# Optimization experiments

Measured on AMD Instinct MI355X. Metric: run time of the kernel, lower is better.

The kernel has to match this reference:

```python
import jax, jax.numpy as jnp
import numpy as np
import math

BS, SEQ, EMBED = 1, 2048, 512
N_HEADS, FEAT = 8, 64
W, DILATION = 32, 4


def setup_inputs() -> dict:
    key = jax.random.key(0)
    ks = jax.random.split(key, 8)
    s = 0.02
    return {
        "x": jax.random.normal(ks[0], (BS, SEQ, EMBED), dtype=jnp.float32),
        "Wq": jax.random.normal(ks[1], (EMBED, N_HEADS * FEAT), dtype=jnp.float32) * s,
        "Wk": jax.random.normal(ks[2], (EMBED, N_HEADS * FEAT), dtype=jnp.float32) * s,
        "Wv": jax.random.normal(ks[3], (EMBED, N_HEADS * FEAT), dtype=jnp.float32) * s,
        "Wff1": jax.random.normal(ks[4], (EMBED, EMBED), dtype=jnp.float32) * s,
        "bff1": jnp.zeros((EMBED,), dtype=jnp.float32),
        "Wff2": jax.random.normal(ks[5], (EMBED, EMBED), dtype=jnp.float32) * s,
        "bff2": jnp.zeros((EMBED,), dtype=jnp.float32),
    }


def reference(x, Wq, Wk, Wv, Wff1, bff1, Wff2, bff2):
    bs, seq, embed = x.shape
    sqrt_d = math.sqrt(FEAT)

    def proj_heads(W):
        # (bs, seq, embed) @ (embed, h*f) -> (bs, h, seq, f)
        h = jnp.einsum('bse,ef->bsf', x, W)
        return h.reshape(bs, seq, N_HEADS, FEAT).transpose(0, 2, 1, 3)

    q = proj_heads(Wq)
    k = proj_heads(Wk)
    v = proj_heads(Wv)

    pad = W * DILATION
    pad_k = jnp.pad(k, ((0, 0), (0, 0), (pad, pad), (0, 0)))
    pad_v = jnp.pad(v, ((0, 0), (0, 0), (pad, pad), (0, 0)))

    # dilated window indices into the padded sequence: (seq, 2W+1)
    idx = jnp.arange(seq)[:, None] + jnp.arange(0, 2 * W * DILATION + 1, DILATION)[None, :]

    diag_k = pad_k[:, :, idx, :]               # (bs, h, seq, 2W+1, f)
    attn = jnp.einsum('bhsf,bhskf->bhsk', q, diag_k)
    # Faithful to source: softmax first, THEN divide by sqrt(d)
    attn = jax.nn.softmax(attn, axis=-1) / sqrt_d
    diag_v = pad_v[:, :, idx, :]               # (bs, h, seq, 2W+1, f)
    ctx = jnp.einsum('bhsk,bhskf->bhsf', attn, diag_v)

    x_attn = ctx.transpose(0, 2, 1, 3).reshape(bs, seq, embed)
    f = jax.nn.relu(x_attn @ Wff1 + bff1)
    g = jax.nn.relu(f @ Wff2 + bff2)
    return x_attn + g
```

## Files before the change

kernel.cpp:

```cpp
#include <hip/hip_runtime.h>
#include <hip/hip_bf16.h>

#define SEQ 2048
#define EMB 512

typedef __attribute__((ext_vector_type(8))) short short8;
typedef __attribute__((ext_vector_type(4))) float f32x4;

__device__ __forceinline__ ushort f2b(float f) {
    union { __hip_bfloat16 h; ushort u; } cv;
    cv.h = __float2bfloat16(f);
    return cv.u;
}

__device__ __forceinline__ void async_copy16(const void* g, void* l) {
    __builtin_amdgcn_global_load_lds(
        (const __attribute__((address_space(1))) void*)g,
        (__attribute__((address_space(3))) void*)l, 16, 0, 0);
}

__global__ __launch_bounds__(256)
void cvt_x(const float* __restrict__ x, ushort* __restrict__ xb) {
    int i = (blockIdx.x * 256 + threadIdx.x) * 4;
    float4 v = *(const float4*)(x + i);
    ushort4 o;
    o.x = f2b(v.x); o.y = f2b(v.y); o.z = f2b(v.z); o.w = f2b(v.w);
    *(ushort4*)(xb + i) = o;
}

__global__ __launch_bounds__(256)
void transpose_w(const float* W0, const float* W1, const float* W2,
                 const float* W3, const float* W4,
                 ushort* T0, ushort* T1, ushort* T2, ushort* T3, ushort* T4) {
    const float* W; ushort* T;
    switch (blockIdx.z) {
        case 0: W = W0; T = T0; break;
        case 1: W = W1; T = T1; break;
        case 2: W = W2; T = T2; break;
        case 3: W = W3; T = T3; break;
        default: W = W4; T = T4; break;
    }
    __shared__ float t[32][33];
    const int n0 = blockIdx.x * 32, k0 = blockIdx.y * 32;
    const int tx = threadIdx.x, ty = threadIdx.y;
    for (int r = ty; r < 32; r += 8)
        t[r][tx] = W[(k0 + r) * 512 + n0 + tx];
    __syncthreads();
    for (int r = ty; r < 32; r += 8)
        T[(n0 + r) * 512 + k0 + tx] = f2b(t[tx][r]);
}

template<bool BIAS, bool RELU, bool ADDSRC, bool OUTBF16>
__global__ __launch_bounds__(256)
void gemm_bt(const ushort* __restrict__ A, const ushort* __restrict__ BT,
             const float* __restrict__ bias, const float* __restrict__ addsrc,
             void* __restrict__ C, int ldc)
{
    __shared__ __align__(16) ushort As[2][64][64];
    __shared__ __align__(16) ushort Bs[2][64][64];
    const int tid = threadIdx.x;
    const int wv = tid >> 6, lane = tid & 63;
    const int lane15 = lane & 15, quad = lane >> 4;
    const int n0 = blockIdx.x * 64, m0 = blockIdx.y * 64;
    const int wm = wv & 1, wn = wv >> 1;
    const int srow = lane >> 3;
    const int soct = lane & 7;

    f32x4 acc[2][2];
    const f32x4 z4 = {0.f, 0.f, 0.f, 0.f};
    acc[0][0] = z4; acc[0][1] = z4; acc[1][0] = z4; acc[1][1] = z4;

    auto stage = [&](int buf, int kc) {
        #pragma unroll
        for (int half = 0; half < 2; ++half) {
            int r0 = wv * 16 + half * 8;
            int r  = r0 + srow;
            int g  = soct ^ (r & 7);
            async_copy16(A + (size_t)(m0 + r) * 512 + kc * 64 + g * 8,
                         &As[buf][r0][0]);
            async_copy16(BT + (size_t)(n0 + r) * 512 + kc * 64 + g * 8,
                         &Bs[buf][r0][0]);
        }
    };
    auto compute = [&](int buf) {
        #pragma unroll
        for (int ks = 0; ks < 2; ++ks) {
            short8 a[2], b[2];
            const int oct = ((ks * 4 + quad) ^ (lane15 & 7)) * 8;
            #pragma unroll
            for (int mi = 0; mi < 2; ++mi)
                a[mi] = *(const short8*)&As[buf][wm * 32 + mi * 16 + lane15][oct];
            #pragma unroll
            for (int ni = 0; ni < 2; ++ni)
                b[ni] = *(const short8*)&Bs[buf][wn * 32 + ni * 16 + lane15][oct];
            #pragma unroll
            for (int mi = 0; mi < 2; ++mi)
                #pragma unroll
                for (int ni = 0; ni < 2; ++ni)
                    acc[mi][ni] = __builtin_amdgcn_mfma_f32_16x16x32_bf16(
                        a[mi], b[ni], acc[mi][ni], 0, 0, 0);
        }
    };

    stage(0, 0);
    __syncthreads();
    for (int kc = 0; kc < 8; ++kc) {
        if (kc < 7) stage((kc + 1) & 1, kc + 1);
        compute(kc & 1);
        __syncthreads();
    }

    #pragma unroll
    for (int mi = 0; mi < 2; ++mi)
        #pragma unroll
        for (int ni = 0; ni < 2; ++ni)
            #pragma unroll
            for (int reg = 0; reg < 4; ++reg) {
                int row = m0 + wm * 32 + mi * 16 + quad * 4 + reg;
                int col = n0 + wn * 32 + ni * 16 + lane15;
                float v = acc[mi][ni][reg];
                if (BIAS) v += bias[col];
                if (RELU) v = fmaxf(v, 0.f);
                if (ADDSRC) v += addsrc[(size_t)row * ldc + col];
                if (OUTBF16) ((ushort*)C)[(size_t)row * ldc + col] = f2b(v);
                else         ((float*)C)[(size_t)row * ldc + col] = v;
            }
}

__global__ __launch_bounds__(256)
void vt_transpose(const ushort* __restrict__ QKVb, ushort* __restrict__ Vtg)
{
    const int sb = blockIdx.x, h = blockIdx.y;
    const int s0 = sb * 64;
    const int tid = threadIdx.x;
    __shared__ ushort tile[64][72];
    #pragma unroll
    for (int it = 0; it < 2; ++it) {
        int row = (tid >> 3) + 32 * it;
        int o = tid & 7;
        *(short8*)&tile[row][o * 8] =
            *(const short8*)&QKVb[(size_t)(s0 + row) * 1536 + 1024 + h * 64 + o * 8];
    }
    __syncthreads();
    const int f = tid >> 2, r = tid & 3;
    ushort tmp[16];
    #pragma unroll
    for (int k = 0; k < 16; ++k) tmp[k] = tile[4 * k + r][f];
    size_t base = (((size_t)h * 4 + r) * 64 + f) * 512 + s0 / 4;
    *(short8*)&Vtg[base]     = *(short8*)&tmp[0];
    *(short8*)&Vtg[base + 8] = *(short8*)&tmp[8];
}

__global__ __launch_bounds__(256)
void attn_kernel(const ushort* __restrict__ QKVb, const ushort* __restrict__ Vtg,
                 float* __restrict__ X, ushort* __restrict__ Xb)
{
    const int c = blockIdx.x, r = blockIdx.y, h = blockIdx.z;
    const int tid = threadIdx.x;
    const int wv = tid >> 6, lane = tid & 63;
    const int lane15 = lane & 15, quad = lane >> 4;
    const int s0 = r + 128 * c;
    const int wm = wv & 1, nh = wv >> 1;

    __shared__ __align__(16) ushort Qs[32][64];
    __shared__ __align__(16) ushort Ks[96][64];
    __shared__ __align__(16) ushort Vts[64][128];
    __shared__ __align__(16) ushort Ps[32][128];
    __shared__ float psum[2][32];

    {
        int i = tid >> 3, o = tid & 7, g = o ^ (i & 7);
        *(short8*)&Qs[i][o * 8] =
            *(const short8*)&QKVb[(size_t)(s0 + 4 * i) * 1536 + h * 64 + g * 8];
    }
    #pragma unroll
    for (int j = 0; j < 3; ++j) {
        int row = (tid >> 3) + 32 * j;
        int o = tid & 7, g = o ^ (row & 7);
        int p = s0 - 128 + 4 * row;
        short8 v = {0, 0, 0, 0, 0, 0, 0, 0};
        if (p >= 0 && p < SEQ)
            v = *(const short8*)&QKVb[(size_t)p * 1536 + 512 + h * 64 + g * 8];
        *(short8*)&Ks[row][o * 8] = v;
    }
    {
        const int u0 = 32 * c - 32;
        const int f = tid & 63;
        #pragma unroll
        for (int j = 0; j < 3; ++j) {
            int o = (tid >> 6) + 4 * j;
            int u = u0 + 8 * o;
            short8 v = {0, 0, 0, 0, 0, 0, 0, 0};
            if (u >= 0 && u < 512)
                v = *(const short8*)&Vtg[(((size_t)h * 4 + r) * 64 + f) * 512 + u];
            *(short8*)&Vts[f][(o ^ (f & 7)) * 8] = v;
        }
    }
    __syncthreads();

    f32x4 lacc[3];
    const f32x4 z4 = {0.f, 0.f, 0.f, 0.f};
    lacc[0] = z4; lacc[1] = z4; lacc[2] = z4;
    short8 qa[2];
    #pragma unroll
    for (int kt = 0; kt < 2; ++kt)
        qa[kt] = *(const short8*)
            &Qs[wm * 16 + lane15][((kt * 4 + quad) ^ (lane15 & 7)) * 8];
    #pragma unroll
    for (int tt = 0; tt < 3; ++tt) {
        int nt = 3 * nh + tt;
        #pragma unroll
        for (int kt = 0; kt < 2; ++kt) {
            short8 kb = *(const short8*)
                &Ks[nt * 16 + lane15][((kt * 4 + quad) ^ (lane15 & 7)) * 8];
            lacc[tt] = __builtin_amdgcn_mfma_f32_16x16x32_bf16(qa[kt], kb, lacc[tt], 0, 0, 0);
        }
    }

    const int rowi = wm * 16 + quad * 4;
    float part[4] = {0.f, 0.f, 0.f, 0.f};
    #pragma unroll
    for (int tt = 0; tt < 3; ++tt) {
        int t = (3 * nh + tt) * 16 + lane15;
        #pragma unroll
        for (int reg = 0; reg < 4; ++reg) {
            int i = rowi + reg;
            int d = t - i;
            float e = 0.f;
            if (d >= 0 && d <= 64) e = __expf(lacc[tt][reg]);
            part[reg] += e;
            int ol = (t >> 3) ^ (i & 7);
            Ps[i][ol * 8 + (t & 7)] = f2b(e);
        }
    }
    #pragma unroll
    for (int reg = 0; reg < 4; ++reg) {
        float v = part[reg];
        v += __shfl_xor(v, 1);
        v += __shfl_xor(v, 2);
        v += __shfl_xor(v, 4);
        v += __shfl_xor(v, 8);
        part[reg] = v;
    }
    if (lane15 == 0) {
        #pragma unroll
        for (int reg = 0; reg < 4; ++reg)
            psum[nh][rowi + reg] = part[reg];
    }
    __syncthreads();

    f32x4 oacc[2];
    oacc[0] = z4; oacc[1] = z4;
    short8 pa[3];
    #pragma unroll
    for (int kc = 0; kc < 3; ++kc)
        pa[kc] = *(const short8*)
            &Ps[wm * 16 + lane15][((kc * 4 + quad) ^ (lane15 & 7)) * 8];
    #pragma unroll
    for (int ft = 0; ft < 2; ++ft) {
        int fr = (2 * nh + ft) * 16 + lane15;
        #pragma unroll
        for (int kc = 0; kc < 3; ++kc) {
            short8 vb = *(const short8*)
                &Vts[fr][((kc * 4 + quad) ^ (fr & 7)) * 8];
            oacc[ft] = __builtin_amdgcn_mfma_f32_16x16x32_bf16(pa[kc], vb, oacc[ft], 0, 0, 0);
        }
    }

    #pragma unroll
    for (int reg = 0; reg < 4; ++reg) {
        int i = rowi + reg;
        float inv = 0.125f / (psum[0][i] + psum[1][i]);
        #pragma unroll
        for (int ft = 0; ft < 2; ++ft) {
            int f = (2 * nh + ft) * 16 + lane15;
            float v = oacc[ft][reg] * inv;
            size_t idx = (size_t)(s0 + 4 * i) * 512 + h * 64 + f;
            X[idx] = v;
            Xb[idx] = f2b(v);
        }
    }
}

extern "C" void kernel_launch(void* const* d_in, const int* in_sizes, int n_in,
                              void* d_out, int out_size, void* d_ws, size_t ws_size,
                              hipStream_t stream)
{
    const float* x    = (const float*)d_in[0];
    const float* Wq   = (const float*)d_in[1];
    const float* Wk   = (const float*)d_in[2];
    const float* Wv   = (const float*)d_in[3];
    const float* Wff1 = (const float*)d_in[4];
    const float* bff1 = (const float*)d_in[5];
    const float* Wff2 = (const float*)d_in[6];
    const float* bff2 = (const float*)d_in[7];
    float* out = (float*)d_out;

    char* w = (char*)d_ws;
    ushort* xb    = (ushort*)(w);
    ushort* WqkvT = (ushort*)(w + (2ull  << 20));
    ushort* W1T   = (ushort*)(w + (3584ull << 10));
    ushort* W2T   = (ushort*)(w + (4ull  << 20));
    ushort* QKVb  = (ushort*)(w + (5ull  << 20));
    ushort* Vtg   = (ushort*)(w + (11ull << 20));
    float*  X     = (float*) (w + (13ull << 20));
    ushort* Xb    = (ushort*)(w + (17ull << 20));
    ushort* Fb    = (ushort*)(w + (19ull << 20));

    cvt_x<<<SEQ * EMB / 1024, 256, 0, stream>>>(x, xb);
    transpose_w<<<dim3(16, 16, 5), dim3(32, 8), 0, stream>>>(
        Wq, Wk, Wv, Wff1, Wff2,
        WqkvT, WqkvT + 512 * 512, WqkvT + 1024 * 512, W1T, W2T);

    gemm_bt<false, false, false, true><<<dim3(24, 32), 256, 0, stream>>>(
        xb, WqkvT, nullptr, nullptr, QKVb, 1536);

    vt_transpose<<<dim3(32, 8), 256, 0, stream>>>(QKVb, Vtg);

    attn_kernel<<<dim3(16, 4, 8), 256, 0, stream>>>(QKVb, Vtg, X, Xb);

    gemm_bt<true, true, false, true><<<dim3(8, 32), 256, 0, stream>>>(
        Xb, W1T, bff1, nullptr, Fb, 512);
    gemm_bt<true, true, true, false><<<dim3(8, 32), 256, 0, stream>>>(
        Fb, W2T, bff2, X, out, 512);
}
```

Baseline: 110.0 us.

## Fuse all stages into one persistent cooperative kernel with grid syncs

```diff
diff --git a/kernel.cpp b/kernel.cpp
--- a/kernel.cpp
+++ b/kernel.cpp
@@ -1,8 +1,10 @@
 #include <hip/hip_runtime.h>
 #include <hip/hip_bf16.h>
+#include <hip/hip_cooperative_groups.h>
+
+namespace cg = cooperative_groups;
 
 #define SEQ 2048
-#define EMB 512
 
 typedef __attribute__((ext_vector_type(8))) short short8;
 typedef __attribute__((ext_vector_type(4))) float f32x4;
@@ -19,86 +21,36 @@
         (__attribute__((address_space(3))) void*)l, 16, 0, 0);
 }
 
-__global__ __launch_bounds__(256)
-void cvt_x(const float* __restrict__ x, ushort* __restrict__ xb) {
-    int i = (blockIdx.x * 256 + threadIdx.x) * 4;
-    float4 v = *(const float4*)(x + i);
-    ushort4 o;
-    o.x = f2b(v.x); o.y = f2b(v.y); o.z = f2b(v.z); o.w = f2b(v.w);
-    *(ushort4*)(xb + i) = o;
-}
-
-__global__ __launch_bounds__(256)
-void transpose_w(const float* W0, const float* W1, const float* W2,
-                 const float* W3, const float* W4,
-                 ushort* T0, ushort* T1, ushort* T2, ushort* T3, ushort* T4) {
-    const float* W; ushort* T;
-    switch (blockIdx.z) {
-        case 0: W = W0; T = T0; break;
-        case 1: W = W1; T = T1; break;
-        case 2: W = W2; T = T2; break;
-        case 3: W = W3; T = T3; break;
-        default: W = W4; T = T4; break;
-    }
-    __shared__ float t[32][33];
-    const int n0 = blockIdx.x * 32, k0 = blockIdx.y * 32;
-    const int tx = threadIdx.x, ty = threadIdx.y;
-    for (int r = ty; r < 32; r += 8)
-        t[r][tx] = W[(k0 + r) * 512 + n0 + tx];
-    __syncthreads();
-    for (int r = ty; r < 32; r += 8)
-        T[(n0 + r) * 512 + k0 + tx] = f2b(t[tx][r]);
-}
-
 template<bool BIAS, bool RELU, bool ADDSRC, bool OUTBF16>
-__global__ __launch_bounds__(256)
-void gemm_bt(const ushort* __restrict__ A, const ushort* __restrict__ BT,
-             const float* __restrict__ bias, const float* __restrict__ addsrc,
-             void* __restrict__ C, int ldc)
+__device__ __forceinline__
+void ffn_tile(char* smem, int b, int tid, const ushort* __restrict__ A,
+              const ushort* __restrict__ BT, const float* __restrict__ bias,
+              const float* __restrict__ addsrc, void* __restrict__ C)
 {
-    __shared__ __align__(16) ushort As[2][64][64];
-    __shared__ __align__(16) ushort Bs[2][64][64];
-    const int tid = threadIdx.x;
     const int wv = tid >> 6, lane = tid & 63;
     const int lane15 = lane & 15, quad = lane >> 4;
-    const int n0 = blockIdx.x * 64, m0 = blockIdx.y * 64;
+    const int srow = lane >> 3, soct = lane & 7;
     const int wm = wv & 1, wn = wv >> 1;
-    const int srow = lane >> 3;
-    const int soct = lane & 7;
-
-    f32x4 acc[2][2];
+    const int n0 = (b & 7) * 64, m0 = (b >> 3) * 32;
+
     const f32x4 z4 = {0.f, 0.f, 0.f, 0.f};
-    acc[0][0] = z4; acc[0][1] = z4; acc[1][0] = z4; acc[1][1] = z4;
+    f32x4 acc[2] = {z4, z4};
 
     auto stage = [&](int buf, int kc) {
+        {
+            int r0 = wv * 8;
+            int r  = r0 + srow;
+            int g  = soct ^ (r & 7);
+            async_copy16(A + (size_t)(m0 + r) * 512 + kc * 64 + g * 8,
+                         smem + buf * 12288 + r0 * 128);
+        }
         #pragma unroll
         for (int half = 0; half < 2; ++half) {
             int r0 = wv * 16 + half * 8;
             int r  = r0 + srow;
             int g  = soct ^ (r & 7);
-            async_copy16(A + (size_t)(m0 + r) * 512 + kc * 64 + g * 8,
-                         &As[buf][r0][0]);
             async_copy16(BT + (size_t)(n0 + r) * 512 + kc * 64 + g * 8,
-                         &Bs[buf][r0][0]);
-        }
-    };
-    auto compute = [&](int buf) {
-        #pragma unroll
-        for (int ks = 0; ks < 2; ++ks) {
-            short8 a[2], b[2];
-            const int oct = ((ks * 4 + quad) ^ (lane15 & 7)) * 8;
-            #pragma unroll
-            for (int mi = 0; mi < 2; ++mi)
-                a[mi] = *(const short8*)&As[buf][wm * 32 + mi * 16 + lane15][oct];
-            #pragma unroll
-            for (int ni = 0; ni < 2; ++ni)
-                b[ni] = *(const short8*)&Bs[buf][wn * 32 + ni * 16 + lane15][oct];
-            #pragma unroll
-            for (int mi = 0; mi < 2; ++mi)
-                #pragma unroll
-                for (int ni = 0; ni < 2; ++ni)
-                    acc[mi][ni] = __builtin_amdgcn_mfma_f32_16x16x32_bf16(
-                        a[mi], b[ni], acc[mi][ni], 0, 0, 0);
+                         smem + buf * 12288 + 4096 + r0 * 128);
         }
     };
 
@@ -106,180 +58,304 @@
     __syncthreads();
     for (int kc = 0; kc < 8; ++kc) {
         if (kc < 7) stage((kc + 1) & 1, kc + 1);
-        compute(kc & 1);
+        const ushort* As = (const ushort*)(smem + (kc & 1) * 12288);
+        const ushort* Bs = As + 2048;
+        #pragma unroll
+        for (int ks = 0; ks < 2; ++ks) {
+            const int oct = ((ks * 4 + quad) ^ (lane15 & 7)) * 8;
+            short8 a = *(const short8*)&As[(wm * 16 + lane15) * 64 + oct];
+            #pragma unroll
+            for (int ni = 0; ni < 2; ++ni) {
+                short8 bb = *(const short8*)&Bs[(wn * 32 + ni * 16 + lane15) * 64 + oct];
+                acc[ni] = __builtin_amdgcn_mfma_f32_16x16x32_bf16(a, bb, acc[ni], 0, 0, 0);
+            }
+        }
         __syncthreads();
     }
 
     #pragma unroll
-    for (int mi = 0; mi < 2; ++mi)
-        #pragma unroll
-        for (int ni = 0; ni < 2; ++ni)
-            #pragma unroll
-            for (int reg = 0; reg < 4; ++reg) {
-                int row = m0 + wm * 32 + mi * 16 + quad * 4 + reg;
-                int col = n0 + wn * 32 + ni * 16 + lane15;
-                float v = acc[mi][ni][reg];
-                if (BIAS) v += bias[col];
-                if (RELU) v = fmaxf(v, 0.f);
-                if (ADDSRC) v += addsrc[(size_t)row * ldc + col];
-                if (OUTBF16) ((ushort*)C)[(size_t)row * ldc + col] = f2b(v);
-                else         ((float*)C)[(size_t)row * ldc + col] = v;
-            }
-}
-
-__global__ __launch_bounds__(256)
-void vt_transpose(const ushort* __restrict__ QKVb, ushort* __restrict__ Vtg)
+    for (int ni = 0; ni < 2; ++ni)
+        #pragma unroll
+        for (int reg = 0; reg < 4; ++reg) {
+            int row = m0 + wm * 16 + quad * 4 + reg;
+            int col = n0 + wn * 32 + ni * 16 + lane15;
+            float v = acc[ni][reg];
+            if (BIAS) v += bias[col];
+            if (RELU) v = fmaxf(v, 0.f);
+            if (ADDSRC) v += addsrc[(size_t)row * 512 + col];
+            if (OUTBF16) ((ushort*)C)[(size_t)row * 512 + col] = f2b(v);
+            else         ((float*)C)[(size_t)row * 512 + col]  = v;
+        }
+}
+
+__global__ __launch_bounds__(256, 2)
+void fused(const float* __restrict__ x,
+           const float* __restrict__ Wq, const float* __restrict__ Wk,
+           const float* __restrict__ Wv, const float* __restrict__ Wff1,
+           const float* __restrict__ bff1, const float* __restrict__ Wff2,
+           const float* __restrict__ bff2,
+           ushort* __restrict__ xb, ushort* __restrict__ WT,
+           ushort* __restrict__ W1T, ushort* __restrict__ W2T,
+           ushort* __restrict__ QKb, ushort* __restrict__ Vtg,
+           float* __restrict__ X, ushort* __restrict__ Xb,
+           ushort* __restrict__ Fb, float* __restrict__ out)
 {
-    const int sb = blockIdx.x, h = blockIdx.y;
-    const int s0 = sb * 64;
+    cg::grid_group grid = cg::this_grid();
+    __shared__ __align__(16) char smem[41216];
     const int tid = threadIdx.x;
-    __shared__ ushort tile[64][72];
-    #pragma unroll
-    for (int it = 0; it < 2; ++it) {
-        int row = (tid >> 3) + 32 * it;
-        int o = tid & 7;
-        *(short8*)&tile[row][o * 8] =
-            *(const short8*)&QKVb[(size_t)(s0 + row) * 1536 + 1024 + h * 64 + o * 8];
-    }
-    __syncthreads();
-    const int f = tid >> 2, r = tid & 3;
-    ushort tmp[16];
-    #pragma unroll
-    for (int k = 0; k < 16; ++k) tmp[k] = tile[4 * k + r][f];
-    size_t base = (((size_t)h * 4 + r) * 64 + f) * 512 + s0 / 4;
-    *(short8*)&Vtg[base]     = *(short8*)&tmp[0];
-    *(short8*)&Vtg[base + 8] = *(short8*)&tmp[8];
-}
-
-__global__ __launch_bounds__(256)
-void attn_kernel(const ushort* __restrict__ QKVb, const ushort* __restrict__ Vtg,
-                 float* __restrict__ X, ushort* __restrict__ Xb)
-{
-    const int c = blockIdx.x, r = blockIdx.y, h = blockIdx.z;
-    const int tid = threadIdx.x;
+    const int b = blockIdx.x;
     const int wv = tid >> 6, lane = tid & 63;
     const int lane15 = lane & 15, quad = lane >> 4;
-    const int s0 = r + 128 * c;
-    const int wm = wv & 1, nh = wv >> 1;
-
-    __shared__ __align__(16) ushort Qs[32][64];
-    __shared__ __align__(16) ushort Ks[96][64];
-    __shared__ __align__(16) ushort Vts[64][128];
-    __shared__ __align__(16) ushort Ps[32][128];
-    __shared__ float psum[2][32];
+    const int srow = lane >> 3, soct = lane & 7;
 
     {
-        int i = tid >> 3, o = tid & 7, g = o ^ (i & 7);
-        *(short8*)&Qs[i][o * 8] =
-            *(const short8*)&QKVb[(size_t)(s0 + 4 * i) * 1536 + h * 64 + g * 8];
+        int t0 = b * 256 + tid;
+        #pragma unroll
+        for (int j = 0; j < 2; ++j) {
+            int i = (t0 + j * 131072) * 4;
+            float4 v = *(const float4*)(x + i);
+            ushort4 o;
+            o.x = f2b(v.x); o.y = f2b(v.y); o.z = f2b(v.z); o.w = f2b(v.w);
+            *(ushort4*)(xb + i) = o;
+        }
+        float (*tsh)[33] = (float(*)[33])smem;
+        const int tx = tid & 31, ty = tid >> 5;
+        for (int j = b; j < 1280; j += 512) {
+            int z = j >> 8, tile = j & 255;
+            const float* W = (z == 0) ? Wq : (z == 1) ? Wk : (z == 2) ? Wv
+                              : (z == 3) ? Wff1 : Wff2;
+            ushort* T = (z == 0) ? WT : (z == 1) ? (WT + 262144)
+                          : (z == 2) ? (WT + 524288) : (z == 3) ? W1T : W2T;
+            int n0 = (tile & 15) * 32, k0 = (tile >> 4) * 32;
+            __syncthreads();
+            for (int r = ty; r < 32; r += 8)
+                tsh[r][tx] = W[(k0 + r) * 512 + n0 + tx];
+            __syncthreads();
+            for (int r = ty; r < 32; r += 8)
+                T[(n0 + r) * 512 + k0 + tx] = f2b(tsh[tx][r]);
+        }
     }
-    #pragma unroll
-    for (int j = 0; j < 3; ++j) {
-        int row = (tid >> 3) + 32 * j;
-        int o = tid & 7, g = o ^ (row & 7);
-        int p = s0 - 128 + 4 * row;
-        short8 v = {0, 0, 0, 0, 0, 0, 0, 0};
-        if (p >= 0 && p < SEQ)
-            v = *(const short8*)&QKVb[(size_t)p * 1536 + 512 + h * 64 + g * 8];
-        *(short8*)&Ks[row][o * 8] = v;
+    grid.sync();
+
+    {
+        ushort* As = (ushort*)smem;
+        ushort* Bs = (ushort*)(smem + 16384);
+        const int wm = wv & 1, wn = wv >> 1;
+        for (int t = b; t < 768; t += 512) {
+            const int nt = t % 24, mt = t / 24;
+            const int n0 = nt * 64, m0 = mt * 64;
+            const ushort* Bt = WT + (size_t)n0 * 512;
+            const f32x4 z4 = {0.f, 0.f, 0.f, 0.f};
+            f32x4 acc[2][2];
+            acc[0][0] = z4; acc[0][1] = z4; acc[1][0] = z4; acc[1][1] = z4;
+
+            auto stage = [&](int buf, int kc) {
+                #pragma unroll
+                for (int half = 0; half < 2; ++half) {
+                    int r0 = wv * 16 + half * 8;
+                    int r  = r0 + srow;
+                    int g  = soct ^ (r & 7);
+                    async_copy16(xb + (size_t)(m0 + r) * 512 + kc * 64 + g * 8,
+                                 As + buf * 4096 + r0 * 64);
+                    async_copy16(Bt + (size_t)r * 512 + kc * 64 + g * 8,
+                                 Bs + buf * 4096 + r0 * 64);
+                }
+            };
+
+            stage(0, 0);
+            __syncthreads();
+            for (int kc = 0; kc < 8; ++kc) {
+                if (kc < 7) stage((kc + 1) & 1, kc + 1);
+                const ushort* Ab = As + (kc & 1) * 4096;
+                const ushort* Bb = Bs + (kc & 1) * 4096;
+                #pragma unroll
+                for (int ks = 0; ks < 2; ++ks) {
+                    const int oct = ((ks * 4 + quad) ^ (lane15 & 7)) * 8;
+                    short8 a[2], bb[2];
+                    #pragma unroll
+                    for (int mi = 0; mi < 2; ++mi)
+                        a[mi] = *(const short8*)&Ab[(wm * 32 + mi * 16 + lane15) * 64 + oct];
+                    #pragma unroll
+                    for (int ni = 0; ni < 2; ++ni)
+                        bb[ni] = *(const short8*)&Bb[(wn * 32 + ni * 16 + lane15) * 64 + oct];
+                    #pragma unroll
+                    for (int mi = 0; mi < 2; ++mi)
+                        #pragma unroll
+                        for (int ni = 0; ni < 2; ++ni)
+                            acc[mi][ni] = __builtin_amdgcn_mfma_f32_16x16x32_bf16(
+                                a[mi], bb[ni], acc[mi][ni], 0, 0, 0);
+                }
+                __syncthreads();
+            }
+
+            if (nt < 16) {
+                #pragma unroll
+                for (int mi = 0; mi < 2; ++mi)
+                    #pragma unroll
+                    for (int ni = 0; ni < 2; ++ni)
+                        #pragma unroll
+                        for (int reg = 0; reg < 4; ++reg) {
+                            int row = m0 + wm * 32 + mi * 16 + quad * 4 + reg;
+                            int col = n0 + wn * 32 + ni * 16 + lane15;
+                            QKb[(size_t)row * 1024 + col] = f2b(acc[mi][ni][reg]);
+                        }
+            } else {
+                const int h = nt - 16;
+                ushort* Ct = (ushort*)smem;
+                #pragma unroll
+                for (int mi = 0; mi < 2; ++mi)
+                    #pragma unroll
+                    for (int ni = 0; ni < 2; ++ni)
+                        #pragma unroll
+                        for (int reg = 0; reg < 4; ++reg) {
+                            int row = wm * 32 + mi * 16 + quad * 4 + reg;
+                            int col = wn * 32 + ni * 16 + lane15;
+                            Ct[row * 64 + col] = f2b(acc[mi][ni][reg]);
+                        }
+                __syncthreads();
+                const int rr = wv, f = lane;
+                __align__(16) ushort tmp[16];
+                #pragma unroll
+                for (int ul = 0; ul < 16; ++ul)
+                    tmp[ul] = Ct[(4 * ul + rr) * 64 + f];
+                size_t base = (((size_t)h * 4 + rr) * 64 + f) * 512 + (m0 >> 2);
+                *(short8*)&Vtg[base]     = *(short8*)&tmp[0];
+                *(short8*)&Vtg[base + 8] = *(short8*)&tmp[8];
+                __syncthreads();
+            }
+        }
     }
+    grid.sync();
+
     {
-        const int u0 = 32 * c - 32;
-        const int f = tid & 63;
+        const int c = b & 15, r = (b >> 4) & 3, h = b >> 6;
+        ushort (*Qs)[64]   = (ushort(*)[64])smem;
+        ushort (*Ks)[64]   = (ushort(*)[64])(smem + 4096);
+        ushort (*Vts)[128] = (ushort(*)[128])(smem + 16384);
+        ushort (*Ps)[128]  = (ushort(*)[128])(smem + 32768);
+        float  (*psum)[32] = (float(*)[32])(smem + 40960);
+        const int s0 = r + 128 * c;
+        const int qwm = wv & 1, qnh = wv >> 1;
+
+        {
+            int i = tid >> 3, o = tid & 7, g = o ^ (i & 7);
+            *(short8*)&Qs[i][o * 8] =
+                *(const short8*)&QKb[(size_t)(s0 + 4 * i) * 1024 + h * 64 + g * 8];
+        }
         #pragma unroll
         for (int j = 0; j < 3; ++j) {
-            int o = (tid >> 6) + 4 * j;
-            int u = u0 + 8 * o;
+            int row = (tid >> 3) + 32 * j;
+            int o = tid & 7, g = o ^ (row & 7);
+            int p = s0 - 128 + 4 * row;
             short8 v = {0, 0, 0, 0, 0, 0, 0, 0};
-            if (u >= 0 && u < 512)
-                v = *(const short8*)&Vtg[(((size_t)h * 4 + r) * 64 + f) * 512 + u];
-            *(short8*)&Vts[f][(o ^ (f & 7)) * 8] = v;
-        }
-    }
-    __syncthreads();
-
-    f32x4 lacc[3];
-    const f32x4 z4 = {0.f, 0.f, 0.f, 0.f};
-    lacc[0] = z4; lacc[1] = z4; lacc[2] = z4;
-    short8 qa[2];
-    #pragma unroll
-    for (int kt = 0; kt < 2; ++kt)
-        qa[kt] = *(const short8*)
-            &Qs[wm * 16 + lane15][((kt * 4 + quad) ^ (lane15 & 7)) * 8];
-    #pragma unroll
-    for (int tt = 0; tt < 3; ++tt) {
-        int nt = 3 * nh + tt;
-        #pragma unroll
-        for (int kt = 0; kt < 2; ++kt) {
-            short8 kb = *(const short8*)
-                &Ks[nt * 16 + lane15][((kt * 4 + quad) ^ (lane15 & 7)) * 8];
-            lacc[tt] = __builtin_amdgcn_mfma_f32_16x16x32_bf16(qa[kt], kb, lacc[tt], 0, 0, 0);
-        }
-    }
-
-    const int rowi = wm * 16 + quad * 4;
-    float part[4] = {0.f, 0.f, 0.f, 0.f};
-    #pragma unroll
-    for (int tt = 0; tt < 3; ++tt) {
-        int t = (3 * nh + tt) * 16 + lane15;
+            if (p >= 0 && p < SEQ)
+                v = *(const short8*)&QKb[(size_t)p * 1024 + 512 + h * 64 + g * 8];
+            *(short8*)&Ks[row][o * 8] = v;
+        }
+        {
+            const int u0 = 32 * c - 32;
+            const int f = tid & 63;
+            #pragma unroll
+            for (int j = 0; j < 3; ++j) {
+                int o = (tid >> 6) + 4 * j;
+                int u = u0 + 8 * o;
+                short8 v = {0, 0, 0, 0, 0, 0, 0, 0};
+                if (u >= 0 && u < 512)
+                    v = *(const short8*)&Vtg[(((size_t)h * 4 + r) * 64 + f) * 512 + u];
+                *(short8*)&Vts[f][(o ^ (f & 7)) * 8] = v;
+            }
+        }
+        __syncthreads();
+
+        const f32x4 z4 = {0.f, 0.f, 0.f, 0.f};
+        f32x4 lacc[3];
+        lacc[0] = z4; lacc[1] = z4; lacc[2] = z4;
+        short8 qa[2];
+        #pragma unroll
+        for (int kt = 0; kt < 2; ++kt)
+            qa[kt] = *(const short8*)
+                &Qs[qwm * 16 + lane15][((kt * 4 + quad) ^ (lane15 & 7)) * 8];
+        #pragma unroll
+        for (int tt = 0; tt < 3; ++tt) {
+            int ntl = 3 * qnh + tt;
+            #pragma unroll
+            for (int kt = 0; kt < 2; ++kt) {
+                short8 kb = *(const short8*)
+                    &Ks[ntl * 16 + lane15][((kt * 4 + quad) ^ (lane15 & 7)) * 8];
+                lacc[tt] = __builtin_amdgcn_mfma_f32_16x16x32_bf16(qa[kt], kb, lacc[tt], 0, 0, 0);
+            }
+        }
+
+        const int rowi = qwm * 16 + quad * 4;
+        float part[4] = {0.f, 0.f, 0.f, 0.f};
+        #pragma unroll
+        for (int tt = 0; tt < 3; ++tt) {
+            int t = (3 * qnh + tt) * 16 + lane15;
+            #pragma unroll
+            for (int reg = 0; reg < 4; ++reg) {
+                int i = rowi + reg;
+                int d = t - i;
+                float e = 0.f;
+                if (d >= 0 && d <= 64) e = __expf(lacc[tt][reg]);
+                part[reg] += e;
+                int ol = (t >> 3) ^ (i & 7);
+                Ps[i][ol * 8 + (t & 7)] = f2b(e);
+            }
+        }
+        #pragma unroll
+        for (int reg = 0; reg < 4; ++reg) {
+            float v = part[reg];
+            v += __shfl_xor(v, 1);
+            v += __shfl_xor(v, 2);
+            v += __shfl_xor(v, 4);
+            v += __shfl_xor(v, 8);
+            part[reg] = v;
+        }
+        if (lane15 == 0) {
+            #pragma unroll
+            for (int reg = 0; reg < 4; ++reg)
+                psum[qnh][rowi + reg] = part[reg];
+        }
+        __syncthreads();
+
+        f32x4 oacc[2];
+        oacc[0] = z4; oacc[1] = z4;
+        short8 pa[3];
+        #pragma unroll
+        for (int kc = 0; kc < 3; ++kc)
+            pa[kc] = *(const short8*)
+                &Ps[qwm * 16 + lane15][((kc * 4 + quad) ^ (lane15 & 7)) * 8];
+        #pragma unroll
+        for (int ft = 0; ft < 2; ++ft) {
+            int fr = (2 * qnh + ft) * 16 + lane15;
+            #pragma unroll
+            for (int kc = 0; kc < 3; ++kc) {
+                short8 vb = *(const short8*)
+                    &Vts[fr][((kc * 4 + quad) ^ (fr & 7)) * 8];
+                oacc[ft] = __builtin_amdgcn_mfma_f32_16x16x32_bf16(pa[kc], vb, oacc[ft], 0, 0, 0);
+            }
+        }
+
         #pragma unroll
         for (int reg = 0; reg < 4; ++reg) {
             int i = rowi + reg;
-            int d = t - i;
-            float e = 0.f;
-            if (d >= 0 && d <= 64) e = __expf(lacc[tt][reg]);
-            part[reg] += e;
-            int ol = (t >> 3) ^ (i & 7);
-            Ps[i][ol * 8 + (t & 7)] = f2b(e);
+            float inv = 0.125f / (psum[0][i] + psum[1][i]);
+            #pragma unroll
+            for (int ft = 0; ft < 2; ++ft) {
+                int f = (2 * qnh + ft) * 16 + lane15;
+                float v = oacc[ft][reg] * inv;
+                size_t idx = (size_t)(s0 + 4 * i) * 512 + h * 64 + f;
+                X[idx]  = v;
+                Xb[idx] = f2b(v);
+            }
         }
     }
-    #pragma unroll
-    for (int reg = 0; reg < 4; ++reg) {
-        float v = part[reg];
-        v += __shfl_xor(v, 1);
-        v += __shfl_xor(v, 2);
-        v += __shfl_xor(v, 4);
-        v += __shfl_xor(v, 8);
-        part[reg] = v;
-    }
-    if (lane15 == 0) {
-        #pragma unroll
-        for (int reg = 0; reg < 4; ++reg)
-            psum[nh][rowi + reg] = part[reg];
-    }
-    __syncthreads();
-
-    f32x4 oacc[2];
-    oacc[0] = z4; oacc[1] = z4;
-    short8 pa[3];
-    #pragma unroll
-    for (int kc = 0; kc < 3; ++kc)
-        pa[kc] = *(const short8*)
-            &Ps[wm * 16 + lane15][((kc * 4 + quad) ^ (lane15 & 7)) * 8];
-    #pragma unroll
-    for (int ft = 0; ft < 2; ++ft) {
-        int fr = (2 * nh + ft) * 16 + lane15;
-        #pragma unroll
-        for (int kc = 0; kc < 3; ++kc) {
-            short8 vb = *(const short8*)
-                &Vts[fr][((kc * 4 + quad) ^ (fr & 7)) * 8];
-            oacc[ft] = __builtin_amdgcn_mfma_f32_16x16x32_bf16(pa[kc], vb, oacc[ft], 0, 0, 0);
-        }
-    }
-
-    #pragma unroll
-    for (int reg = 0; reg < 4; ++reg) {
-        int i = rowi + reg;
-        float inv = 0.125f / (psum[0][i] + psum[1][i]);
-        #pragma unroll
-        for (int ft = 0; ft < 2; ++ft) {
-            int f = (2 * nh + ft) * 16 + lane15;
-            float v = oacc[ft][reg] * inv;
-            size_t idx = (size_t)(s0 + 4 * i) * 512 + h * 64 + f;
-            X[idx] = v;
-            Xb[idx] = f2b(v);
-        }
-    }
+    grid.sync();
+
+    ffn_tile<true, true, false, true>((char*)smem, b, tid, Xb, W1T, bff1, nullptr, Fb);
+    grid.sync();
+
+    ffn_tile<true, true, true, false>((char*)smem, b, tid, Fb, W2T, bff2, X, out);
 }
 
 extern "C" void kernel_launch(void* const* d_in, const int* in_sizes, int n_in,
@@ -297,30 +373,21 @@
     float* out = (float*)d_out;
 
     char* w = (char*)d_ws;
-    ushort* xb    = (ushort*)(w);
-    ushort* WqkvT = (ushort*)(w + (2ull  << 20));
-    ushort* W1T   = (ushort*)(w + (3584ull << 10));
-    ushort* W2T   = (ushort*)(w + (4ull  << 20));
-    ushort* QKVb  = (ushort*)(w + (5ull  << 20));
-    ushort* Vtg   = (ushort*)(w + (11ull << 20));
-    float*  X     = (float*) (w + (13ull << 20));
-    ushort* Xb    = (ushort*)(w + (17ull << 20));
-    ushort* Fb    = (ushort*)(w + (19ull << 20));
-
-    cvt_x<<<SEQ * EMB / 1024, 256, 0, stream>>>(x, xb);
-    transpose_w<<<dim3(16, 16, 5), dim3(32, 8), 0, stream>>>(
-        Wq, Wk, Wv, Wff1, Wff2,
-        WqkvT, WqkvT + 512 * 512, WqkvT + 1024 * 512, W1T, W2T);
-
-    gemm_bt<false, false, false, true><<<dim3(24, 32), 256, 0, stream>>>(
-        xb, WqkvT, nullptr, nullptr, QKVb, 1536);
-
-    vt_transpose<<<dim3(32, 8), 256, 0, stream>>>(QKVb, Vtg);
-
-    attn_kernel<<<dim3(16, 4, 8), 256, 0, stream>>>(QKVb, Vtg, X, Xb);
-
-    gemm_bt<true, true, false, true><<<dim3(8, 32), 256, 0, stream>>>(
-        Xb, W1T, bff1, nullptr, Fb, 512);
-    gemm_bt<true, true, true, false><<<dim3(8, 32), 256, 0, stream>>>(
-        Fb, W2T, bff2, X, out, 512);
-}
+    ushort* xb  = (ushort*)(w);
+    ushort* WT  = (ushort*)(w + (2ull  << 20));
+    ushort* W1T = (ushort*)(w + (3584ull << 10));
+    ushort* W2T = (ushort*)(w + (4ull  << 20));
+    ushort* QKb = (ushort*)(w + (5ull  << 20));
+    ushort* Vtg = (ushort*)(w + (9ull  << 20));
+    float*  X   = (float*) (w + (11ull << 20));
+    ushort* Xb  = (ushort*)(w + (15ull << 20));
+    ushort* Fb  = (ushort*)(w + (17ull << 20));
+
+    void* args[] = { (void*)&x, (void*)&Wq, (void*)&Wk, (void*)&Wv,
+                     (void*)&Wff1, (void*)&bff1, (void*)&Wff2, (void*)&bff2,
+                     (void*)&xb, (void*)&WT, (void*)&W1T, (void*)&W2T,
+                     (void*)&QKb, (void*)&Vtg, (void*)&X, (void*)&Xb,
+                     (void*)&Fb, (void*)&out };
+    hipLaunchCooperativeKernel((void*)fused, dim3(512), dim3(256),
+                               args, 0, stream);
+}
```

Result: slower. 359.5 us (+226.9%).
